# Kernel optimization log

Measured on AMD Instinct MI355X. Metric: run time of the kernel, lower is better.

The kernel has to match this reference:

```python
import jax, jax.numpy as jnp
import numpy as np

N_NODES = 50000
IN_DIM = 256
EDGE_DIM = 128
OUT_DIM = 128
EDGE_OUT_DIM = 128
N_EDGES = 1600000
NEG_SLOPE = 0.01


def leaky_relu(x):
    return jnp.where(x >= 0, x, NEG_SLOPE * x)


def _kaiming(key, out_d, in_d):
    # kaiming_uniform with a=0.01, leaky_relu gain
    gain = np.sqrt(2.0 / (1.0 + 0.01 ** 2))
    bound = gain * np.sqrt(3.0 / in_d)
    return jax.random.uniform(key, (out_d, in_d), jnp.float32, -bound, bound)


def setup_inputs() -> dict:
    key = jax.random.key(0)
    ks = jax.random.split(key, 9)
    x = jax.random.normal(ks[0], (N_NODES, IN_DIM), jnp.float32)
    edge_index = jax.random.randint(ks[1], (2, N_EDGES), 0, N_NODES, jnp.int64)
    edge_attr = jax.random.normal(ks[2], (N_EDGES, EDGE_DIM), jnp.float32)
    W_e = _kaiming(ks[3], OUT_DIM, EDGE_DIM)
    W_hu = _kaiming(ks[4], OUT_DIM, IN_DIM)
    W_hw = _kaiming(ks[5], OUT_DIM, IN_DIM)
    W2 = _kaiming(ks[6], OUT_DIM, IN_DIM)
    W_emb = _kaiming(ks[7], OUT_DIM, IN_DIM)
    W_attr = _kaiming(ks[8], EDGE_OUT_DIM, OUT_DIM)
    return {"x": x, "edge_index": edge_index, "edge_attr": edge_attr,
            "W_e": W_e, "W_hu": W_hu, "W_hw": W_hw,
            "W2": W2, "W_emb": W_emb, "W_attr": W_attr}


def reference(x, edge_index, edge_attr, W_e, W_hu, W_hw, W2, W_emb, W_attr):
    src, tgt = edge_index[0], edge_index[1]
    # project node features once (N x d), then gather per edge -> avoids E-sized GEMMs
    hu = x @ W_hu.T   # [N, out]
    hw = x @ W_hw.T   # [N, out]
    messages = leaky_relu(edge_attr @ W_e.T + hu[src] + hw[tgt])  # [E, out]
    # scatter_mean over target nodes
    sums = jax.ops.segment_sum(messages, tgt, num_segments=N_NODES)
    counts = jax.ops.segment_sum(jnp.ones((messages.shape[0],), messages.dtype), tgt,
                                 num_segments=N_NODES)
    agg = sums / jnp.maximum(counts, 1.0)[:, None]  # zeros where no incoming edges
    attributes = messages @ W_attr.T  # [E, edge_out]
    embeddings = x @ W_emb.T + leaky_relu(x @ W2.T + agg)  # [N, out]
    return embeddings, attributes
```

## Files before the change

### kernel.cpp

```cpp
#include <hip/hip_runtime.h>

#define NN 50000
#define NE 1600000

using bf16x8 = __bf16 __attribute__((ext_vector_type(8)));
using bf16x4 = __bf16 __attribute__((ext_vector_type(4)));
using bf16x2 = __bf16 __attribute__((ext_vector_type(2)));
using f32x4  = float  __attribute__((ext_vector_type(4)));

__device__ __forceinline__ char* swzp(void* base, int row, int byteoff) {
  return (char*)base + (byteoff ^ ((row & 7) << 4));
}
__device__ __forceinline__ const char* swzpc(const void* base, int row, int byteoff) {
  return (const char*)base + (byteoff ^ ((row & 7) << 4));
}

__device__ __forceinline__ int ld_idx(const void* p, int f64, long long i) {
  return f64 ? (int)((const long long*)p)[i] : ((const int*)p)[i];
}

__global__ void detect_idx64(const int* ei32, int* flag) {
  __shared__ int anynz;
  if (threadIdx.x == 0) anynz = 0;
  __syncthreads();
  if (ei32[2 * threadIdx.x + 1] != 0) atomicOr(&anynz, 1);
  __syncthreads();
  if (threadIdx.x == 0) *flag = (anynz == 0) ? 1 : 0;
}

__global__ void prep_weights(const float* We, const float* Whu, const float* Whw,
                             const float* W2, const float* Wemb, const float* Wattr,
                             __bf16* wHUW, __bf16* wET2, __bf16* wE, __bf16* wA) {
  int i = blockIdx.x * 256 + threadIdx.x;
  if (i < 65536) {
    int n = i >> 8, k = i & 255;
    wHUW[i] = (__bf16)(n < 128 ? Whu[n * 256 + k] : Whw[(n - 128) * 256 + k]);
  } else if (i < 131072) {
    int j = i - 65536; int n = j >> 8, k = j & 255;
    wET2[j] = (__bf16)(n < 128 ? Wemb[n * 256 + k] : W2[(n - 128) * 256 + k]);
  } else if (i < 147456) {
    int j = i - 131072; wE[j] = (__bf16)We[j];
  } else {
    int j = i - 147456; wA[j] = (__bf16)Wattr[j];
  }
}

__global__ void k_hist(const void* ei, const int* flag, int* cnt) {
  int i = blockIdx.x * 256 + threadIdx.x;
  int t = ld_idx(ei, *flag, (long long)NE + i);
  atomicAdd(&cnt[t], 1);
}

__global__ void k_part(const int* cnt, int* part) {
  __shared__ int red[256];
  int i = blockIdx.x * 256 + threadIdx.x;
  red[threadIdx.x] = (i < NN) ? cnt[i] : 0;
  __syncthreads();
  for (int s = 128; s > 0; s >>= 1) {
    if (threadIdx.x < s) red[threadIdx.x] += red[threadIdx.x + s];
    __syncthreads();
  }
  if (threadIdx.x == 0) part[blockIdx.x] = red[0];
}

__global__ void k_scanpart(int* part, int n) {
  __shared__ int sc[256];
  int v = (threadIdx.x < n) ? part[threadIdx.x] : 0;
  sc[threadIdx.x] = v;
  __syncthreads();
  for (int d = 1; d < 256; d <<= 1) {
    int add = (threadIdx.x >= d) ? sc[threadIdx.x - d] : 0;
    __syncthreads();
    sc[threadIdx.x] += add;
    __syncthreads();
  }
  if (threadIdx.x < n) part[threadIdx.x] = sc[threadIdx.x] - v;
}

__global__ void k_offsets(const int* cnt, const int* part, int* offs) {
  __shared__ int sc[256];
  int i = blockIdx.x * 256 + threadIdx.x;
  int v = (i < NN) ? cnt[i] : 0;
  sc[threadIdx.x] = v;
  __syncthreads();
  for (int d = 1; d < 256; d <<= 1) {
    int add = (threadIdx.x >= d) ? sc[threadIdx.x - d] : 0;
    __syncthreads();
    sc[threadIdx.x] += add;
    __syncthreads();
  }
  if (i < NN) offs[i] = part[blockIdx.x] + sc[threadIdx.x] - v;
}

__global__ void k_scatter(const void* ei, const int* flag, const int* offs,
                          int* fill, int* perm) {
  int i = blockIdx.x * 256 + threadIdx.x;
  int t = ld_idx(ei, *flag, (long long)NE + i);
  int pos = offs[t] + atomicAdd(&fill[t], 1);
  perm[pos] = i;
}

template <int MODE>
__global__ __launch_bounds__(512) void node_gemm(
    const float* __restrict__ x, const __bf16* __restrict__ W,
    __bf16* __restrict__ hu, __bf16* __restrict__ hw,
    const float* __restrict__ sums, const int* __restrict__ cnt,
    float* __restrict__ out) {
  __shared__ __bf16 sW[256 * 256];
  const int t = threadIdx.x;
  const int lane = t & 63;
  const int w = t >> 6;
  const int h = lane >> 4;
  const int l15 = lane & 15;

  for (int i = t; i < 8192; i += 512) {
    int row = i >> 5, c8 = (i & 31) << 3;
    bf16x8 v = *(const bf16x8*)(W + row * 256 + c8);
    *(bf16x8*)swzp(sW, row, row * 512 + (c8 << 1)) = v;
  }
  __syncthreads();

  const int ntiles = (NN + 127) / 128;
  for (int tile = blockIdx.x; tile < ntiles; tile += gridDim.x) {
    int m0 = tile * 128 + w * 16;
    if (m0 >= NN) continue;
    int node = m0 + l15;

    f32x4 acc[16];
#pragma unroll
    for (int n = 0; n < 16; ++n) { acc[n][0] = 0.f; acc[n][1] = 0.f; acc[n][2] = 0.f; acc[n][3] = 0.f; }

#pragma unroll
    for (int kc = 0; kc < 8; ++kc) {
      const float* xp = x + (long long)node * 256 + kc * 32 + h * 8;
      f32x4 fa = *(const f32x4*)xp;
      f32x4 fb = *(const f32x4*)(xp + 4);
      bf16x8 b;
#pragma unroll
      for (int j = 0; j < 4; ++j) { b[j] = (__bf16)fa[j]; b[j + 4] = (__bf16)fb[j]; }
#pragma unroll
      for (int n = 0; n < 16; ++n) {
        int row = n * 16 + l15;
        bf16x8 a = *(const bf16x8*)swzpc(sW, row, row * 512 + kc * 64 + h * 16);
        acc[n] = __builtin_amdgcn_mfma_f32_16x16x32_bf16(a, b, acc[n], 0, 0, 0);
      }
    }

    if (MODE == 0) {
#pragma unroll
      for (int n = 0; n < 16; ++n) {
        bf16x4 mv;
#pragma unroll
        for (int j = 0; j < 4; ++j) mv[j] = (__bf16)acc[n][j];
        __bf16* dst = (n < 8) ? (hu + (long long)node * 128 + n * 16 + h * 4)
                              : (hw + (long long)node * 128 + (n - 8) * 16 + h * 4);
        *(bf16x4*)dst = mv;
      }
    } else {
      float inv = 1.f / fmaxf((float)cnt[node], 1.0f);
#pragma unroll
      for (int n = 0; n < 8; ++n) {
        f32x4 ag = *(const f32x4*)(sums + (long long)node * 128 + n * 16 + h * 4);
        f32x4 o;
#pragma unroll
        for (int j = 0; j < 4; ++j) {
          float z = acc[n + 8][j] + ag[j] * inv;
          float lr = z >= 0.f ? z : 0.01f * z;
          o[j] = acc[n][j] + lr;
        }
        *(f32x4*)(out + (long long)node * 128 + n * 16 + h * 4) = o;
      }
    }
  }
}

__global__ __launch_bounds__(1024) void edge_fused(
    const float* __restrict__ eattr, const void* __restrict__ ei,
    const int* __restrict__ flag, const int* __restrict__ perm,
    const __bf16* __restrict__ wE, const __bf16* __restrict__ wA,
    const __bf16* __restrict__ hu, const __bf16* __restrict__ hw,
    float* __restrict__ sums, float* __restrict__ attr_out) {
  __shared__ __bf16 sW1[128 * 128];
  __shared__ __bf16 sW2[128 * 128];
  __shared__ __bf16 sM[256 * 128];
  __shared__ int sPerm[2][256], sSrc[2][256], sTgt[2][256];

  const int t = threadIdx.x;
  const int lane = t & 63;
  const int w = t >> 6;
  const int h = lane >> 4;
  const int l15 = lane & 15;
  const int f = *flag;

  for (int i = t; i < 2048; i += 1024) {
    int row = i >> 4, c8 = (i & 15) << 3;
    bf16x8 v1 = *(const bf16x8*)(wE + row * 128 + c8);
    bf16x8 v2 = *(const bf16x8*)(wA + row * 128 + c8);
    int b = row * 256 + (c8 << 1);
    *(bf16x8*)swzp(sW1, row, b) = v1;
    *(bf16x8*)swzp(sW2, row, b) = v2;
  }

  const int ntiles = NE / 256;
  int cur = 0;
  if (blockIdx.x < ntiles && t < 256) {
    int p = perm[blockIdx.x * 256 + t];
    sPerm[0][t] = p;
    sSrc[0][t] = ld_idx(ei, f, p);
    sTgt[0][t] = ld_idx(ei, f, (long long)NE + p);
  }

  for (int tile = blockIdx.x; tile < ntiles; tile += gridDim.x) {
    __syncthreads();

    const int myP = sPerm[cur][w * 16 + l15];
    const int tgtI = sTgt[cur][w * 16 + l15];
    const float* ep = eattr + (long long)myP * 128 + h * 8;
    f32x4 fa[4], fb[4];
#pragma unroll
    for (int kc = 0; kc < 4; ++kc) {
      fa[kc] = *(const f32x4*)(ep + kc * 32);
      fb[kc] = *(const f32x4*)(ep + kc * 32 + 4);
    }

    for (int i = t; i < 4096; i += 1024) {
      int r = i >> 4, c8 = (i & 15) << 3;
      bf16x8 a = *(const bf16x8*)(hu + (long long)sSrc[cur][r] * 128 + c8);
      bf16x8 b = *(const bf16x8*)(hw + (long long)sTgt[cur][r] * 128 + c8);
      bf16x8 o;
#pragma unroll
      for (int j = 0; j < 8; ++j) o[j] = (__bf16)((float)a[j] + (float)b[j]);
      *(bf16x8*)swzp(sM, r, r * 256 + (c8 << 1)) = o;
    }

    int ntile = tile + gridDim.x;
    if (ntile < ntiles && t < 256) {
      int pp = perm[ntile * 256 + t];
      sPerm[cur ^ 1][t] = pp;
      sSrc[cur ^ 1][t] = ld_idx(ei, f, pp);
      sTgt[cur ^ 1][t] = ld_idx(ei, f, (long long)NE + pp);
    }
    __syncthreads();

    f32x4 acc[8];
#pragma unroll
    for (int n = 0; n < 8; ++n) { acc[n][0] = 0.f; acc[n][1] = 0.f; acc[n][2] = 0.f; acc[n][3] = 0.f; }
#pragma unroll
    for (int kc = 0; kc < 4; ++kc) {
      bf16x8 bfr;
#pragma unroll
      for (int j = 0; j < 4; ++j) { bfr[j] = (__bf16)fa[kc][j]; bfr[j + 4] = (__bf16)fb[kc][j]; }
#pragma unroll
      for (int n = 0; n < 8; ++n) {
        int row = n * 16 + l15;
        bf16x8 a = *(const bf16x8*)swzpc(sW1, row, row * 256 + kc * 64 + (h << 4));
        acc[n] = __builtin_amdgcn_mfma_f32_16x16x32_bf16(a, bfr, acc[n], 0, 0, 0);
      }
    }

    const int R = w * 16 + l15;
#pragma unroll
    for (int n = 0; n < 8; ++n) {
      __bf16* mp = (__bf16*)swzp(sM, R, R * 256 + n * 32 + h * 8);
      bf16x4 hsv = *(const bf16x4*)mp;
      bf16x4 mv;
#pragma unroll
      for (int j = 0; j < 4; ++j) {
        float z = acc[n][j] + (float)hsv[j];
        float m = z >= 0.f ? z : 0.01f * z;
        mv[j] = (__bf16)m;
      }
      *(bf16x4*)mp = mv;
    }

    {
      float s0 = 0.f, s1 = 0.f;
      int curT = __shfl(tgtI, 0);
#pragma unroll
      for (int r = 0; r < 16; ++r) {
        int tg = __shfl(tgtI, r);
        if (tg != curT) {
          unsafeAtomicAdd(&sums[(long long)curT * 128 + 2 * lane], s0);
          unsafeAtomicAdd(&sums[(long long)curT * 128 + 2 * lane + 1], s1);
          s0 = 0.f; s1 = 0.f; curT = tg;
        }
        int R2 = w * 16 + r;
        bf16x2 v = *(const bf16x2*)swzpc(sM, R2, R2 * 256 + lane * 4);
        s0 += (float)v[0]; s1 += (float)v[1];
      }
      unsafeAtomicAdd(&sums[(long long)curT * 128 + 2 * lane], s0);
      unsafeAtomicAdd(&sums[(long long)curT * 128 + 2 * lane + 1], s1);
    }

    f32x4 acc2[8];
#pragma unroll
    for (int n = 0; n < 8; ++n) { acc2[n][0] = 0.f; acc2[n][1] = 0.f; acc2[n][2] = 0.f; acc2[n][3] = 0.f; }
#pragma unroll
    for (int ks = 0; ks < 4; ++ks) {
      bf16x8 a2 = *(const bf16x8*)swzpc(sM, R, R * 256 + ks * 64 + (h << 4));
#pragma unroll
      for (int nt = 0; nt < 8; ++nt) {
        int row = nt * 16 + l15;
        bf16x8 b2 = *(const bf16x8*)swzpc(sW2, row, row * 256 + ks * 64 + (h << 4));
        acc2[nt] = __builtin_amdgcn_mfma_f32_16x16x32_bf16(a2, b2, acc2[nt], 0, 0, 0);
      }
    }

    int gp[4];
#pragma unroll
    for (int j = 0; j < 4; ++j) gp[j] = __shfl(myP, (h << 2) + j);
#pragma unroll
    for (int nt = 0; nt < 8; ++nt) {
#pragma unroll
      for (int j = 0; j < 4; ++j) {
        attr_out[(long long)gp[j] * 128 + nt * 16 + l15] = acc2[nt][j];
      }
    }

    cur ^= 1;
  }
}

extern "C" void kernel_launch(void* const* d_in, const int* in_sizes, int n_in,
                              void* d_out, int out_size, void* d_ws, size_t ws_size,
                              hipStream_t stream) {
  const float* x     = (const float*)d_in[0];
  const void*  ei    = d_in[1];
  const float* eattr = (const float*)d_in[2];
  const float* We    = (const float*)d_in[3];
  const float* Whu   = (const float*)d_in[4];
  const float* Whw   = (const float*)d_in[5];
  const float* W2    = (const float*)d_in[6];
  const float* Wemb  = (const float*)d_in[7];
  const float* Wattr = (const float*)d_in[8];

  float* out_emb  = (float*)d_out;
  float* out_attr = out_emb + (size_t)NN * 128;

  char* ws = (char*)d_ws;
  float*  sums = (float*)ws;
  int*    cnt  = (int*)(ws + 25600000);
  int*    fill = (int*)(ws + 25800064);
  int*    offs = (int*)(ws + 26000128);
  int*    part = (int*)(ws + 26200192);
  int*    flag = (int*)(ws + 26201216);
  int*    perm = (int*)(ws + 26201280);
  __bf16* hu   = (__bf16*)(ws + 32601280);
  __bf16* hw   = (__bf16*)(ws + 45401280);
  __bf16* wHUW = (__bf16*)(ws + 58201280);
  __bf16* wET2 = wHUW + 65536;
  __bf16* wE   = wET2 + 65536;
  __bf16* wA   = wE + 16384;

  hipMemsetAsync(ws, 0, 26000128, stream);
  detect_idx64<<<1, 1024, 0, stream>>>((const int*)ei, flag);
  prep_weights<<<640, 256, 0, stream>>>(We, Whu, Whw, W2, Wemb, Wattr, wHUW, wET2, wE, wA);
  k_hist<<<6250, 256, 0, stream>>>(ei, flag, cnt);
  k_part<<<196, 256, 0, stream>>>(cnt, part);
  k_scanpart<<<1, 256, 0, stream>>>(part, 196);
  k_offsets<<<196, 256, 0, stream>>>(cnt, part, offs);
  k_scatter<<<6250, 256, 0, stream>>>(ei, flag, offs, fill, perm);
  node_gemm<0><<<391, 512, 0, stream>>>(x, wHUW, hu, hw, nullptr, nullptr, nullptr);
  edge_fused<<<2048, 1024, 0, stream>>>(eattr, ei, flag, perm, wE, wA, hu, hw, sums, out_attr);
  node_gemm<1><<<391, 512, 0, stream>>>(x, wET2, nullptr, nullptr, sums, cnt, out_emb);
}
```

Measured before the change: 792.8 us.

## Warp-specialize edge kernel into producer gather waves and consumer MFMA waves

Splits the 16 waves of edge_fused into 8 producer waves and 8 consumer waves. Producers gather hu/hw rows for the next 128-edge tile into a double-buffered shared tile while consumers run the two MFMA GEMMs, the scatter atomics and the attribute stores on the current tile. The aim is to overlap the random-access gathers with compute and to need only one barrier per tile. In exchange, tiles shrink from 256 to 128 edges and only half the waves do math, and the launch grid is unchanged, so per-block work and MFMA throughput per block may drop.

```diff
diff --git a/kernel.cpp b/kernel.cpp
--- a/kernel.cpp
+++ b/kernel.cpp
@@ -182,8 +182,8 @@
     float* __restrict__ sums, float* __restrict__ attr_out) {
   __shared__ __bf16 sW1[128 * 128];
   __shared__ __bf16 sW2[128 * 128];
-  __shared__ __bf16 sM[256 * 128];
-  __shared__ int sPerm[2][256], sSrc[2][256], sTgt[2][256];
+  __shared__ __bf16 sM[2][128 * 128];
+  __shared__ int sPerm[2][128], sTgt[2][128];
 
   const int t = threadIdx.x;
   const int lane = t & 63;
@@ -191,6 +191,7 @@
   const int h = lane >> 4;
   const int l15 = lane & 15;
   const int f = *flag;
+  const bool producer = (w >= 8);
 
   for (int i = t; i < 2048; i += 1024) {
     int row = i >> 4, c8 = (i & 15) << 3;
@@ -201,123 +202,152 @@
     *(bf16x8*)swzp(sW2, row, b) = v2;
   }
 
-  const int ntiles = NE / 256;
-  int cur = 0;
-  if (blockIdx.x < ntiles && t < 256) {
-    int p = perm[blockIdx.x * 256 + t];
-    sPerm[0][t] = p;
-    sSrc[0][t] = ld_idx(ei, f, p);
-    sTgt[0][t] = ld_idx(ei, f, (long long)NE + p);
-  }
-
-  for (int tile = blockIdx.x; tile < ntiles; tile += gridDim.x) {
-    __syncthreads();
-
-    const int myP = sPerm[cur][w * 16 + l15];
-    const int tgtI = sTgt[cur][w * 16 + l15];
-    const float* ep = eattr + (long long)myP * 128 + h * 8;
-    f32x4 fa[4], fb[4];
-#pragma unroll
-    for (int kc = 0; kc < 4; ++kc) {
-      fa[kc] = *(const f32x4*)(ep + kc * 32);
-      fb[kc] = *(const f32x4*)(ep + kc * 32 + 4);
+  const int ntiles = NE / 128;
+  const int tile0 = blockIdx.x;
+  if (tile0 >= ntiles) return;
+  int buf = 0;
+
+  if (producer) {
+    int q = w - 8;
+    int pr = q * 16 + l15;
+    int p = perm[(long long)tile0 * 128 + pr];
+    int srcI = ld_idx(ei, f, p);
+    int tgtI = ld_idx(ei, f, (long long)NE + p);
+    sPerm[0][pr] = p;
+    sTgt[0][pr] = tgtI;
+#pragma unroll
+    for (int it = 0; it < 4; ++it) {
+      int rr = it * 4 + h;
+      int sR = __shfl(srcI, rr);
+      int tR = __shfl(tgtI, rr);
+      bf16x8 a = *(const bf16x8*)(hu + (long long)sR * 128 + l15 * 8);
+      bf16x8 b = *(const bf16x8*)(hw + (long long)tR * 128 + l15 * 8);
+      bf16x8 o;
+#pragma unroll
+      for (int j = 0; j < 8; ++j) o[j] = (__bf16)((float)a[j] + (float)b[j]);
+      int R = q * 16 + rr;
+      *(bf16x8*)swzp(sM[0], R, R * 256 + l15 * 16) = o;
     }
-
-    for (int i = t; i < 4096; i += 1024) {
-      int r = i >> 4, c8 = (i & 15) << 3;
-      bf16x8 a = *(const bf16x8*)(hu + (long long)sSrc[cur][r] * 128 + c8);
-      bf16x8 b = *(const bf16x8*)(hw + (long long)sTgt[cur][r] * 128 + c8);
-      bf16x8 o;
-#pragma unroll
-      for (int j = 0; j < 8; ++j) o[j] = (__bf16)((float)a[j] + (float)b[j]);
-      *(bf16x8*)swzp(sM, r, r * 256 + (c8 << 1)) = o;
+  }
+  __syncthreads();
+
+  for (int tile = tile0; tile < ntiles; tile += gridDim.x) {
+    int ntile = tile + gridDim.x;
+    bool more = ntile < ntiles;
+
+    if (producer) {
+      if (more) {
+        int q = w - 8;
+        int pr = q * 16 + l15;
+        int p = perm[(long long)ntile * 128 + pr];
+        int srcI = ld_idx(ei, f, p);
+        int tgtI = ld_idx(ei, f, (long long)NE + p);
+        sPerm[buf ^ 1][pr] = p;
+        sTgt[buf ^ 1][pr] = tgtI;
+#pragma unroll
+        for (int it = 0; it < 4; ++it) {
+          int rr = it * 4 + h;
+          int sR = __shfl(srcI, rr);
+          int tR = __shfl(tgtI, rr);
+          bf16x8 a = *(const bf16x8*)(hu + (long long)sR * 128 + l15 * 8);
+          bf16x8 b = *(const bf16x8*)(hw + (long long)tR * 128 + l15 * 8);
+          bf16x8 o;
+#pragma unroll
+          for (int j = 0; j < 8; ++j) o[j] = (__bf16)((float)a[j] + (float)b[j]);
+          int R = q * 16 + rr;
+          *(bf16x8*)swzp(sM[buf ^ 1], R, R * 256 + l15 * 16) = o;
+        }
+      }
+    } else {
+      __bf16* sMb = sM[buf];
+      const int myP = sPerm[buf][w * 16 + l15];
+      const int tgtI = sTgt[buf][w * 16 + l15];
+      const float* ep = eattr + (long long)myP * 128 + h * 8;
+      f32x4 fa[4], fb[4];
+#pragma unroll
+      for (int kc = 0; kc < 4; ++kc) {
+        fa[kc] = *(const f32x4*)(ep + kc * 32);
+        fb[kc] = *(const f32x4*)(ep + kc * 32 + 4);
+      }
+
+      f32x4 acc[8];
+#pragma unroll
+      for (int n = 0; n < 8; ++n) { acc[n][0] = 0.f; acc[n][1] = 0.f; acc[n][2] = 0.f; acc[n][3] = 0.f; }
+#pragma unroll
+      for (int kc = 0; kc < 4; ++kc) {
+        bf16x8 bfr;
+#pragma unroll
+        for (int j = 0; j < 4; ++j) { bfr[j] = (__bf16)fa[kc][j]; bfr[j + 4] = (__bf16)fb[kc][j]; }
+#pragma unroll
+        for (int n = 0; n < 8; ++n) {
+          int row = n * 16 + l15;
+          bf16x8 a = *(const bf16x8*)swzpc(sW1, row, row * 256 + kc * 64 + (h << 4));
+          acc[n] = __builtin_amdgcn_mfma_f32_16x16x32_bf16(a, bfr, acc[n], 0, 0, 0);
+        }
+      }
+
+      const int R = w * 16 + l15;
+#pragma unroll
+      for (int n = 0; n < 8; ++n) {
+        __bf16* mp = (__bf16*)swzp(sMb, R, R * 256 + n * 32 + h * 8);
+        bf16x4 hsv = *(const bf16x4*)mp;
+        bf16x4 mv;
+#pragma unroll
+        for (int j = 0; j < 4; ++j) {
+          float z = acc[n][j] + (float)hsv[j];
+          float m = z >= 0.f ? z : 0.01f * z;
+          mv[j] = (__bf16)m;
+        }
+        *(bf16x4*)mp = mv;
+      }
+
+      {
+        float s0 = 0.f, s1 = 0.f;
+        int curT = __shfl(tgtI, 0);
+#pragma unroll
+        for (int r = 0; r < 16; ++r) {
+          int tg = __shfl(tgtI, r);
+          if (tg != curT) {
+            unsafeAtomicAdd(&sums[(long long)curT * 128 + 2 * lane], s0);
+            unsafeAtomicAdd(&sums[(long long)curT * 128 + 2 * lane + 1], s1);
+            s0 = 0.f; s1 = 0.f; curT = tg;
+          }
+          int R2 = w * 16 + r;
+          bf16x2 v = *(const bf16x2*)swzpc(sMb, R2, R2 * 256 + lane * 4);
+          s0 += (float)v[0]; s1 += (float)v[1];
+        }
+        unsafeAtomicAdd(&sums[(long long)curT * 128 + 2 * lane], s0);
+        unsafeAtomicAdd(&sums[(long long)curT * 128 + 2 * lane + 1], s1);
+      }
+
+      f32x4 acc2[8];
+#pragma unroll
+      for (int n = 0; n < 8; ++n) { acc2[n][0] = 0.f; acc2[n][1] = 0.f; acc2[n][2] = 0.f; acc2[n][3] = 0.f; }
+#pragma unroll
+      for (int ks = 0; ks < 4; ++ks) {
+        bf16x8 a2 = *(const bf16x8*)swzpc(sMb, R, R * 256 + ks * 64 + (h << 4));
+#pragma unroll
+        for (int nt = 0; nt < 8; ++nt) {
+          int row = nt * 16 + l15;
+          bf16x8 b2 = *(const bf16x8*)swzpc(sW2, row, row * 256 + ks * 64 + (h << 4));
+          acc2[nt] = __builtin_amdgcn_mfma_f32_16x16x32_bf16(a2, b2, acc2[nt], 0, 0, 0);
+        }
+      }
+
+      int gp[4];
+#pragma unroll
+      for (int j = 0; j < 4; ++j) gp[j] = __shfl(myP, (h << 2) + j);
+#pragma unroll
+      for (int nt = 0; nt < 8; ++nt) {
+#pragma unroll
+        for (int j = 0; j < 4; ++j) {
+          attr_out[(long long)gp[j] * 128 + nt * 16 + l15] = acc2[nt][j];
+        }
+      }
     }
 
-    int ntile = tile + gridDim.x;
-    if (ntile < ntiles && t < 256) {
-      int pp = perm[ntile * 256 + t];
-      sPerm[cur ^ 1][t] = pp;
-      sSrc[cur ^ 1][t] = ld_idx(ei, f, pp);
-      sTgt[cur ^ 1][t] = ld_idx(ei, f, (long long)NE + pp);
-    }
-    __syncthreads();
-
-    f32x4 acc[8];
-#pragma unroll
-    for (int n = 0; n < 8; ++n) { acc[n][0] = 0.f; acc[n][1] = 0.f; acc[n][2] = 0.f; acc[n][3] = 0.f; }
-#pragma unroll
-    for (int kc = 0; kc < 4; ++kc) {
-      bf16x8 bfr;
-#pragma unroll
-      for (int j = 0; j < 4; ++j) { bfr[j] = (__bf16)fa[kc][j]; bfr[j + 4] = (__bf16)fb[kc][j]; }
-#pragma unroll
-      for (int n = 0; n < 8; ++n) {
-        int row = n * 16 + l15;
-        bf16x8 a = *(const bf16x8*)swzpc(sW1, row, row * 256 + kc * 64 + (h << 4));
-        acc[n] = __builtin_amdgcn_mfma_f32_16x16x32_bf16(a, bfr, acc[n], 0, 0, 0);
-      }
-    }
-
-    const int R = w * 16 + l15;
-#pragma unroll
-    for (int n = 0; n < 8; ++n) {
-      __bf16* mp = (__bf16*)swzp(sM, R, R * 256 + n * 32 + h * 8);
-      bf16x4 hsv = *(const bf16x4*)mp;
-      bf16x4 mv;
-#pragma unroll
-      for (int j = 0; j < 4; ++j) {
-        float z = acc[n][j] + (float)hsv[j];
-        float m = z >= 0.f ? z : 0.01f * z;
-        mv[j] = (__bf16)m;
-      }
-      *(bf16x4*)mp = mv;
-    }
-
-    {
-      float s0 = 0.f, s1 = 0.f;
-      int curT = __shfl(tgtI, 0);
-#pragma unroll
-      for (int r = 0; r < 16; ++r) {
-        int tg = __shfl(tgtI, r);
-        if (tg != curT) {
-          unsafeAtomicAdd(&sums[(long long)curT * 128 + 2 * lane], s0);
-          unsafeAtomicAdd(&sums[(long long)curT * 128 + 2 * lane + 1], s1);
-          s0 = 0.f; s1 = 0.f; curT = tg;
-        }
-        int R2 = w * 16 + r;
-        bf16x2 v = *(const bf16x2*)swzpc(sM, R2, R2 * 256 + lane * 4);
-        s0 += (float)v[0]; s1 += (float)v[1];
-      }
-      unsafeAtomicAdd(&sums[(long long)curT * 128 + 2 * lane], s0);
-      unsafeAtomicAdd(&sums[(long long)curT * 128 + 2 * lane + 1], s1);
-    }
-
-    f32x4 acc2[8];
-#pragma unroll
-    for (int n = 0; n < 8; ++n) { acc2[n][0] = 0.f; acc2[n][1] = 0.f; acc2[n][2] = 0.f; acc2[n][3] = 0.f; }
-#pragma unroll
-    for (int ks = 0; ks < 4; ++ks) {
-      bf16x8 a2 = *(const bf16x8*)swzpc(sM, R, R * 256 + ks * 64 + (h << 4));
-#pragma unroll
-      for (int nt = 0; nt < 8; ++nt) {
-        int row = nt * 16 + l15;
-        bf16x8 b2 = *(const bf16x8*)swzpc(sW2, row, row * 256 + ks * 64 + (h << 4));
-        acc2[nt] = __builtin_amdgcn_mfma_f32_16x16x32_bf16(a2, b2, acc2[nt], 0, 0, 0);
-      }
-    }
-
-    int gp[4];
-#pragma unroll
-    for (int j = 0; j < 4; ++j) gp[j] = __shfl(myP, (h << 2) + j);
-#pragma unroll
-    for (int nt = 0; nt < 8; ++nt) {
-#pragma unroll
-      for (int j = 0; j < 4; ++j) {
-        attr_out[(long long)gp[j] * 128 + nt * 16 + l15] = acc2[nt][j];
-      }
-    }
-
-    cur ^= 1;
+    __syncthreads();
+    buf ^= 1;
   }
 }
 
```

Result: no change. 791.0 us (-0.2%).
